# Performance work log

Hardware: AMD Instinct MI355X
Metric: run time of the kernel (lower is better)

Reference implementation:

```python
import jax, jax.numpy as jnp
import numpy as np

# ---- constants matching init_kwargs ----
NUM_CLASSES = 20
NUM_GRID = 7
NUM_BBOX = 2
IN_SIZE = 448          # image_shapes = (448, 448)
IOU_THRESHOLD = 0.7    # self.num_threshold passed to batched_nms
SCORE_THRESHOLD = 0.1  # boxes[:, -1] > 0.1 reserve mask
M = NUM_GRID * NUM_GRID  # 49 boxes per image
BATCH = 16384


def setup_inputs() -> dict:
    key = jax.random.key(0)
    out_features = M * (NUM_CLASSES + 5 * NUM_BBOX)  # 1470
    x = jax.random.uniform(key, (BATCH, out_features), dtype=jnp.float32)
    return {"x": x}


def _iou_matrix(boxes):
    # boxes: [M, 4] in (x0, y0, x1, y1). Returns [M, M] pairwise IoU.
    area = jnp.clip(boxes[:, 2] - boxes[:, 0], 0) * jnp.clip(boxes[:, 3] - boxes[:, 1], 0)
    lt = jnp.maximum(boxes[:, None, :2], boxes[None, :, :2])   # [M, M, 2]
    rb = jnp.minimum(boxes[:, None, 2:], boxes[None, :, 2:])   # [M, M, 2]
    wh = jnp.clip(rb - lt, 0)
    inter = wh[..., 0] * wh[..., 1]
    union = area[:, None] + area[None, :] - inter
    return inter / jnp.maximum(union, 1e-9)


def _nms_keep(boxes, scores, labels, valid):
    # Per-image class-aware NMS (torchvision batched_nms semantics via coordinate offsets).
    # boxes [M,4], scores [M], labels [M] int, valid [M] bool -> keep mask [M] bool.
    max_coord = jnp.max(boxes)
    offs = labels.astype(boxes.dtype) * (max_coord + 1.0)
    b = boxes + offs[:, None]
    s = jnp.where(valid, scores, -jnp.inf)
    order = jnp.argsort(-s)                 # descending by score, invalid last
    bs = b[order]
    vs = valid[order]
    iou = _iou_matrix(bs)                   # [M, M]
    idx = jnp.arange(M)

    def step(suppressed, i):
        keep_i = vs[i] & ~suppressed[i]
        suppressed = suppressed | (keep_i & (iou[i] > IOU_THRESHOLD) & (idx > i))
        return suppressed, keep_i

    _, keep_sorted = jax.lax.scan(step, jnp.zeros((M,), bool), idx)
    return jnp.zeros((M,), bool).at[order].set(keep_sorted)


def reference(x):
    N = x.shape[0]
    x = x.reshape(N, M, NUM_CLASSES + 5 * NUM_BBOX)
    class_logits = x[..., :NUM_CLASSES]                       # [N, M, C]
    bb = x[..., NUM_CLASSES:].reshape(N, M, NUM_BBOX, 5)      # [N, M, B, 5]
    # pick the bbox with max confidence per cell
    best = jnp.argmax(bb[..., 4], axis=-1)                    # [N, M]
    yolo_bboxes = jnp.take_along_axis(bb, best[..., None, None], axis=2)[:, :, 0, :]  # [N, M, 5]

    probs = jax.nn.softmax(class_logits, axis=-1)
    labels = jnp.argmax(probs, axis=-1)                       # [N, M]

    # boxes_decode: grid offsets (x tiles, y repeats) then cx/cy/w/h -> corners
    g = jnp.arange(NUM_GRID, dtype=x.dtype)
    x_grid = jnp.tile(g, NUM_GRID)                            # [M]
    y_grid = jnp.repeat(g, NUM_GRID)                          # [M]
    cx = (yolo_bboxes[..., 0] + x_grid) / NUM_GRID
    cy = (yolo_bboxes[..., 1] + y_grid) / NUM_GRID
    hw = yolo_bboxes[..., 2] / 2
    hh = yolo_bboxes[..., 3] / 2
    W = jnp.asarray(IN_SIZE, x.dtype)
    H = jnp.asarray(IN_SIZE, x.dtype)
    x0 = (cx - hw) * W
    y0 = (cy - hh) * H
    x1 = (cx + hw) * W
    y1 = (cy + hh) * H
    scores = yolo_bboxes[..., 4]
    reserve_mask = scores > SCORE_THRESHOLD                   # [N, M]

    # clip_boxes_to_image
    x0 = jnp.clip(x0, 0, IN_SIZE); x1 = jnp.clip(x1, 0, IN_SIZE)
    y0 = jnp.clip(y0, 0, IN_SIZE); y1 = jnp.clip(y1, 0, IN_SIZE)
    boxes = jnp.stack([x0, y0, x1, y1], axis=-1)              # [N, M, 4]

    keep_mask = jax.vmap(_nms_keep)(boxes, scores, labels, reserve_mask)  # [N, M]
    return class_logits, yolo_bboxes, boxes, scores, labels, keep_mask, reserve_mask
```

## Files before the change

### kernel.cpp

```cpp
#include <hip/hip_runtime.h>
#include <math.h>

#define NCLS   20
#define MCELLS 49
#define FEAT   30
#define ITEMF  1470

typedef unsigned long long u64;
typedef unsigned int u32;
typedef float f32x4 __attribute__((ext_vector_type(4)));

__device__ __forceinline__ void nts(float* p, float v) { __builtin_nontemporal_store(v, p); }
__device__ __forceinline__ float bperm(int srcLane, float v) {
  return __int_as_float(__builtin_amdgcn_ds_bpermute(srcLane << 2, __float_as_int(v)));
}

__global__ __launch_bounds__(256) void yolo_post(const float* __restrict__ x,
                                                 float* __restrict__ out,
                                                 int N) {
  const int wave = threadIdx.x >> 6;
  const int lane = threadIdx.x & 63;
  const int n = blockIdx.x * 4 + wave;
  if (n >= N) return;

  const float* item = x + (size_t)n * ITEMF;

  const size_t NM = (size_t)N * MCELLS;
  float* out0 = out;
  float* out1 = out0 + NM * 20;
  float* out2 = out1 + NM * 5;
  float* out3 = out2 + NM * 4;
  float* out4 = out3 + NM;
  float* out5 = out4 + NM;
  float* out6 = out5 + NM;

  const int m = lane;
  const bool cellv = (m < MCELLS);

  float2 v[15];
  if (cellv) {
    const float2* Lp = (const float2*)(item + m * FEAT);
#pragma unroll
    for (int j = 0; j < 15; ++j) v[j] = Lp[j];
  } else {
#pragma unroll
    for (int j = 0; j < 15; ++j) v[j] = make_float2(0.f, 0.f);
  }

  {
    float* dst = out0 + (size_t)n * (MCELLS * NCLS);
#pragma unroll
    for (int i = 0; i < 16; ++i) {
      int idx = lane + i * 64;
      if (idx < MCELLS * NCLS) {
        int c = idx / NCLS;
        int k = idx - c * NCLS;
        nts(dst + idx, item[c * FEAT + k]);
      }
    }
  }

  int   labi = 0;
  float conf = 0.f;
  float x0 = 0.f, y0 = 0.f, x1 = 0.f, y1 = 0.f;
  bool  reserve = false;

  if (cellv) {
    float bestv = v[0].x;
    if (v[0].y > bestv) { bestv = v[0].y; labi = 1; }
#pragma unroll
    for (int j = 1; j < 10; ++j) {
      if (v[j].x > bestv) { bestv = v[j].x; labi = 2 * j; }
      if (v[j].y > bestv) { bestv = v[j].y; labi = 2 * j + 1; }
    }

    float c0 = v[12].x, c1 = v[14].y;
    bool sel1 = (c1 > c0);
    float bx = sel1 ? v[12].y : v[10].x;
    float by = sel1 ? v[13].x : v[10].y;
    float bw = sel1 ? v[13].y : v[11].x;
    float bh = sel1 ? v[14].x : v[11].y;
    conf = sel1 ? c1 : c0;

    float xg = (float)(m % 7), yg = (float)(m / 7);
    float cx = (bx + xg) / 7.0f, cy = (by + yg) / 7.0f;
    float hw = bw * 0.5f, hh = bh * 0.5f;
    x0 = fminf(fmaxf((cx - hw) * 448.0f, 0.f), 448.f);
    y0 = fminf(fmaxf((cy - hh) * 448.0f, 0.f), 448.f);
    x1 = fminf(fmaxf((cx + hw) * 448.0f, 0.f), 448.f);
    y1 = fminf(fmaxf((cy + hh) * 448.0f, 0.f), 448.f);
    reserve = (conf > 0.1f);

    size_t ci = (size_t)n * MCELLS + m;
    float* yb = out1 + ci * 5;
    nts(yb + 0, bx); nts(yb + 1, by); nts(yb + 2, bw); nts(yb + 3, bh); nts(yb + 4, conf);
    f32x4 bx4 = { x0, y0, x1, y1 };
    __builtin_nontemporal_store(bx4, (f32x4*)(out2 + ci * 4));
    nts(out3 + ci, conf);
    nts(out4 + ci, (float)labi);
    nts(out6 + ci, reserve ? 1.0f : 0.0f);
  }

  const bool meValid = (cellv && reserve);
  const u64 validb = __ballot(meValid);

  u64 same = ~0ull;
#pragma unroll
  for (int b = 0; b < 5; ++b) {
    u64 bb = __ballot(((labi >> b) & 1) != 0);
    same &= ((labi >> b) & 1) ? bb : ~bb;
  }
  u64 peers = same & validb & ~(1ull << lane);
  if (!meValid) peers = 0;

  int pc = __popcll(peers);
#pragma unroll
  for (int d = 1; d < 64; d <<= 1) {
    int o = __shfl_xor(pc, d);
    pc = pc > o ? pc : o;
  }
  const int T = __builtin_amdgcn_readfirstlane(pc);

  const float area_i = fmaxf(x1 - x0, 0.f) * fmaxf(y1 - y0, 0.f);
  u64 candme = 0;
  u64 rem = peers;
  for (int t = 0; t < T; ++t) {
    int j = rem ? (int)__builtin_ctzll(rem) : lane;
    rem &= rem - 1;
    float cj  = bperm(j, conf);
    float jx0 = bperm(j, x0), jy0 = bperm(j, y0);
    float jx1 = bperm(j, x1), jy1 = bperm(j, y1);
    bool prec = (cj > conf) || ((cj == conf) && (j < lane));
    float aj = fmaxf(jx1 - jx0, 0.f) * fmaxf(jy1 - jy0, 0.f);
    float iw = fminf(jx1, x1) - fmaxf(jx0, x0);
    float ih = fminf(jy1, y1) - fmaxf(jy0, y0);
    float inter = fmaxf(iw, 0.f) * fmaxf(ih, 0.f);
    float uni = aj + area_i - inter;
    bool sup = prec && (inter > 0.7f * fmaxf(uni, 1e-9f));
    candme |= sup ? (1ull << j) : 0ull;
  }

  u64 undecided = validb, kept = 0;
  while (undecided) {
    bool meUnd  = meValid && ((undecided >> lane) & 1ull);
    bool ready  = meUnd && ((candme & undecided) == 0ull);
    u64 readyb  = __ballot(ready);
    u64 keptb   = __ballot(ready && ((candme & kept) == 0ull));
    kept |= keptb;
    undecided &= ~readyb;
  }

  if (cellv) nts(out5 + (size_t)n * MCELLS + m, (float)((kept >> lane) & 1ull));
}

extern "C" void kernel_launch(void* const* d_in, const int* in_sizes, int n_in,
                              void* d_out, int out_size, void* d_ws, size_t ws_size,
                              hipStream_t stream) {
  const float* x = (const float*)d_in[0];
  float* out = (float*)d_out;
  int N = in_sizes[0] / ITEMF;
  int grid = (N + 3) / 4;
  yolo_post<<<grid, 256, 0, stream>>>(x, out, N);
}
```

Measured before the change: 40.52 us.

## Process four images per wave with double-buffered register prefetch

Each wave now handles four images instead of one. The per-cell loads for the next image are issued into a second register buffer before the current image is processed. This is meant to hide global-load latency behind the NMS and store work, and to cut the number of waves launched. In exchange it raises register pressure, which may lower occupancy, and leaves a quarter as many waves to spread across the GPU. Lanes 49 and above no longer zero-initialise the item buffer, but those values are never used.

```diff
diff --git a/kernel.cpp b/kernel.cpp
--- a/kernel.cpp
+++ b/kernel.cpp
@@ -5,6 +5,7 @@
 #define MCELLS 49
 #define FEAT   30
 #define ITEMF  1470
+#define IPW    4
 
 typedef unsigned long long u64;
 typedef unsigned int u32;
@@ -15,37 +16,26 @@
   return __int_as_float(__builtin_amdgcn_ds_bpermute(srcLane << 2, __float_as_int(v)));
 }
 
-__global__ __launch_bounds__(256) void yolo_post(const float* __restrict__ x,
-                                                 float* __restrict__ out,
-                                                 int N) {
-  const int wave = threadIdx.x >> 6;
-  const int lane = threadIdx.x & 63;
-  const int n = blockIdx.x * 4 + wave;
+struct Item { float2 v[15]; };
+
+__device__ __forceinline__ void loadItem(Item& it, const float* __restrict__ x,
+                                         long n, int N, bool cellv, int m) {
+  if ((n < N) && cellv) {
+    const float2* Lp = (const float2*)(x + (size_t)n * ITEMF + m * FEAT);
+#pragma unroll
+    for (int j = 0; j < 15; ++j) it.v[j] = Lp[j];
+  }
+}
+
+__device__ __forceinline__ void processItem(const Item& it, long n, int N, int lane,
+                                            const float* __restrict__ x,
+                                            float* out0, float* out1, float* out2,
+                                            float* out3, float* out4, float* out5,
+                                            float* out6) {
   if (n >= N) return;
-
-  const float* item = x + (size_t)n * ITEMF;
-
-  const size_t NM = (size_t)N * MCELLS;
-  float* out0 = out;
-  float* out1 = out0 + NM * 20;
-  float* out2 = out1 + NM * 5;
-  float* out3 = out2 + NM * 4;
-  float* out4 = out3 + NM;
-  float* out5 = out4 + NM;
-  float* out6 = out5 + NM;
-
   const int m = lane;
   const bool cellv = (m < MCELLS);
-
-  float2 v[15];
-  if (cellv) {
-    const float2* Lp = (const float2*)(item + m * FEAT);
-#pragma unroll
-    for (int j = 0; j < 15; ++j) v[j] = Lp[j];
-  } else {
-#pragma unroll
-    for (int j = 0; j < 15; ++j) v[j] = make_float2(0.f, 0.f);
-  }
+  const float* item = x + (size_t)n * ITEMF;
 
   {
     float* dst = out0 + (size_t)n * (MCELLS * NCLS);
@@ -66,20 +56,20 @@
   bool  reserve = false;
 
   if (cellv) {
-    float bestv = v[0].x;
-    if (v[0].y > bestv) { bestv = v[0].y; labi = 1; }
+    float bestv = it.v[0].x;
+    if (it.v[0].y > bestv) { bestv = it.v[0].y; labi = 1; }
 #pragma unroll
     for (int j = 1; j < 10; ++j) {
-      if (v[j].x > bestv) { bestv = v[j].x; labi = 2 * j; }
-      if (v[j].y > bestv) { bestv = v[j].y; labi = 2 * j + 1; }
+      if (it.v[j].x > bestv) { bestv = it.v[j].x; labi = 2 * j; }
+      if (it.v[j].y > bestv) { bestv = it.v[j].y; labi = 2 * j + 1; }
     }
 
-    float c0 = v[12].x, c1 = v[14].y;
+    float c0 = it.v[12].x, c1 = it.v[14].y;
     bool sel1 = (c1 > c0);
-    float bx = sel1 ? v[12].y : v[10].x;
-    float by = sel1 ? v[13].x : v[10].y;
-    float bw = sel1 ? v[13].y : v[11].x;
-    float bh = sel1 ? v[14].x : v[11].y;
+    float bx = sel1 ? it.v[12].y : it.v[10].x;
+    float by = sel1 ? it.v[13].x : it.v[10].y;
+    float bw = sel1 ? it.v[13].y : it.v[11].x;
+    float bh = sel1 ? it.v[14].x : it.v[11].y;
     conf = sel1 ? c1 : c0;
 
     float xg = (float)(m % 7), yg = (float)(m / 7);
@@ -153,12 +143,45 @@
   if (cellv) nts(out5 + (size_t)n * MCELLS + m, (float)((kept >> lane) & 1ull));
 }
 
+__global__ __launch_bounds__(256) void yolo_post(const float* __restrict__ x,
+                                                 float* __restrict__ out,
+                                                 int N) {
+  const int wave = threadIdx.x >> 6;
+  const int lane = threadIdx.x & 63;
+  const int gw = blockIdx.x * 4 + wave;
+  const long i0 = (long)gw * IPW;
+  if (i0 >= N) return;
+
+  const int m = lane;
+  const bool cellv = (m < MCELLS);
+
+  const size_t NM = (size_t)N * MCELLS;
+  float* out0 = out;
+  float* out1 = out0 + NM * 20;
+  float* out2 = out1 + NM * 5;
+  float* out3 = out2 + NM * 4;
+  float* out4 = out3 + NM;
+  float* out5 = out4 + NM;
+  float* out6 = out5 + NM;
+
+  Item A, B;
+  loadItem(A, x, i0 + 0, N, cellv, m);
+  loadItem(B, x, i0 + 1, N, cellv, m);
+  processItem(A, i0 + 0, N, lane, x, out0, out1, out2, out3, out4, out5, out6);
+  loadItem(A, x, i0 + 2, N, cellv, m);
+  processItem(B, i0 + 1, N, lane, x, out0, out1, out2, out3, out4, out5, out6);
+  loadItem(B, x, i0 + 3, N, cellv, m);
+  processItem(A, i0 + 2, N, lane, x, out0, out1, out2, out3, out4, out5, out6);
+  processItem(B, i0 + 3, N, lane, x, out0, out1, out2, out3, out4, out5, out6);
+}
+
 extern "C" void kernel_launch(void* const* d_in, const int* in_sizes, int n_in,
                               void* d_out, int out_size, void* d_ws, size_t ws_size,
                               hipStream_t stream) {
   const float* x = (const float*)d_in[0];
   float* out = (float*)d_out;
   int N = in_sizes[0] / ITEMF;
-  int grid = (N + 3) / 4;
+  int waves = (N + IPW - 1) / IPW;
+  int grid = (waves + 3) / 4;
   yolo_post<<<grid, 256, 0, stream>>>(x, out, N);
 }
```

After: 50.42 us. 1.24x slower.

## Split into streaming decode kernel and separate NMS kernel, stage logits via LDS

Applied to the files above, without the earlier changes.

Splits the single fused kernel into two. The first streams the input, writes the outputs and stages class logits through shared memory so they are copied from registers rather than re-read from global memory. The second kernel reloads the boxes, scores and labels from the output buffer (regular stores so they stay in cache) and runs the NMS. The goal is to keep the bandwidth-bound phase free of the divergent NMS loops. In exchange it adds a second launch and an extra read pass over the box, score and label data, and the shared-memory staging relies only on a block-level fence within the wave.

```diff
diff --git a/kernel.cpp b/kernel.cpp
--- a/kernel.cpp
+++ b/kernel.cpp
@@ -15,15 +15,16 @@
   return __int_as_float(__builtin_amdgcn_ds_bpermute(srcLane << 2, __float_as_int(v)));
 }
 
-__global__ __launch_bounds__(256) void yolo_post(const float* __restrict__ x,
-                                                 float* __restrict__ out,
-                                                 int N) {
+__global__ __launch_bounds__(256) void yolo_stream(const float* __restrict__ x,
+                                                   float* __restrict__ out,
+                                                   int N) {
   const int wave = threadIdx.x >> 6;
   const int lane = threadIdx.x & 63;
   const int n = blockIdx.x * 4 + wave;
+
+  __shared__ float slog[4][MCELLS * NCLS];
+
   if (n >= N) return;
-
-  const float* item = x + (size_t)n * ITEMF;
 
   const size_t NM = (size_t)N * MCELLS;
   float* out0 = out;
@@ -31,15 +32,14 @@
   float* out2 = out1 + NM * 5;
   float* out3 = out2 + NM * 4;
   float* out4 = out3 + NM;
-  float* out5 = out4 + NM;
-  float* out6 = out5 + NM;
+  float* out6 = out4 + NM * 2;
 
   const int m = lane;
   const bool cellv = (m < MCELLS);
 
   float2 v[15];
   if (cellv) {
-    const float2* Lp = (const float2*)(item + m * FEAT);
+    const float2* Lp = (const float2*)(x + (size_t)n * ITEMF + m * FEAT);
 #pragma unroll
     for (int j = 0; j < 15; ++j) v[j] = Lp[j];
   } else {
@@ -47,25 +47,24 @@
     for (int j = 0; j < 15; ++j) v[j] = make_float2(0.f, 0.f);
   }
 
+  if (cellv) {
+    float2* dst = (float2*)&slog[wave][m * NCLS];
+#pragma unroll
+    for (int j = 0; j < 10; ++j) dst[j] = v[j];
+  }
+  __threadfence_block();
   {
     float* dst = out0 + (size_t)n * (MCELLS * NCLS);
+    const float* s = slog[wave];
 #pragma unroll
     for (int i = 0; i < 16; ++i) {
       int idx = lane + i * 64;
-      if (idx < MCELLS * NCLS) {
-        int c = idx / NCLS;
-        int k = idx - c * NCLS;
-        nts(dst + idx, item[c * FEAT + k]);
-      }
+      if (idx < MCELLS * NCLS) nts(dst + idx, s[idx]);
     }
   }
 
-  int   labi = 0;
-  float conf = 0.f;
-  float x0 = 0.f, y0 = 0.f, x1 = 0.f, y1 = 0.f;
-  bool  reserve = false;
-
   if (cellv) {
+    int labi = 0;
     float bestv = v[0].x;
     if (v[0].y > bestv) { bestv = v[0].y; labi = 1; }
 #pragma unroll
@@ -80,26 +79,52 @@
     float by = sel1 ? v[13].x : v[10].y;
     float bw = sel1 ? v[13].y : v[11].x;
     float bh = sel1 ? v[14].x : v[11].y;
-    conf = sel1 ? c1 : c0;
+    float conf = sel1 ? c1 : c0;
 
     float xg = (float)(m % 7), yg = (float)(m / 7);
     float cx = (bx + xg) / 7.0f, cy = (by + yg) / 7.0f;
     float hw = bw * 0.5f, hh = bh * 0.5f;
-    x0 = fminf(fmaxf((cx - hw) * 448.0f, 0.f), 448.f);
-    y0 = fminf(fmaxf((cy - hh) * 448.0f, 0.f), 448.f);
-    x1 = fminf(fmaxf((cx + hw) * 448.0f, 0.f), 448.f);
-    y1 = fminf(fmaxf((cy + hh) * 448.0f, 0.f), 448.f);
-    reserve = (conf > 0.1f);
+    float x0 = fminf(fmaxf((cx - hw) * 448.0f, 0.f), 448.f);
+    float y0 = fminf(fmaxf((cy - hh) * 448.0f, 0.f), 448.f);
+    float x1 = fminf(fmaxf((cx + hw) * 448.0f, 0.f), 448.f);
+    float y1 = fminf(fmaxf((cy + hh) * 448.0f, 0.f), 448.f);
 
     size_t ci = (size_t)n * MCELLS + m;
     float* yb = out1 + ci * 5;
     nts(yb + 0, bx); nts(yb + 1, by); nts(yb + 2, bw); nts(yb + 3, bh); nts(yb + 4, conf);
     f32x4 bx4 = { x0, y0, x1, y1 };
-    __builtin_nontemporal_store(bx4, (f32x4*)(out2 + ci * 4));
-    nts(out3 + ci, conf);
-    nts(out4 + ci, (float)labi);
-    nts(out6 + ci, reserve ? 1.0f : 0.0f);
+    *(f32x4*)(out2 + ci * 4) = bx4;
+    out3[ci] = conf;
+    out4[ci] = (float)labi;
+    nts(out6 + ci, (conf > 0.1f) ? 1.0f : 0.0f);
   }
+}
+
+__global__ __launch_bounds__(256) void yolo_nms(float* __restrict__ out, int N) {
+  const int wave = threadIdx.x >> 6;
+  const int lane = threadIdx.x & 63;
+  const int n = blockIdx.x * 4 + wave;
+  if (n >= N) return;
+
+  const size_t NM = (size_t)N * MCELLS;
+  const float* out2 = out + NM * 25;
+  const float* out3 = out + NM * 29;
+  const float* out4 = out + NM * 30;
+  float* out5 = out + NM * 31;
+
+  const int m = lane;
+  const bool cellv = (m < MCELLS);
+  const size_t ci = (size_t)n * MCELLS + m;
+
+  float x0 = 0.f, y0 = 0.f, x1 = 0.f, y1 = 0.f, conf = 0.f;
+  int labi = 0;
+  if (cellv) {
+    f32x4 b = *(const f32x4*)(out2 + ci * 4);
+    x0 = b.x; y0 = b.y; x1 = b.z; y1 = b.w;
+    conf = out3[ci];
+    labi = (int)out4[ci];
+  }
+  const bool reserve = (conf > 0.1f);
 
   const bool meValid = (cellv && reserve);
   const u64 validb = __ballot(meValid);
@@ -150,7 +175,7 @@
     undecided &= ~readyb;
   }
 
-  if (cellv) nts(out5 + (size_t)n * MCELLS + m, (float)((kept >> lane) & 1ull));
+  if (cellv) nts(out5 + ci, (float)((kept >> lane) & 1ull));
 }
 
 extern "C" void kernel_launch(void* const* d_in, const int* in_sizes, int n_in,
@@ -160,5 +185,6 @@
   float* out = (float*)d_out;
   int N = in_sizes[0] / ITEMF;
   int grid = (N + 3) / 4;
-  yolo_post<<<grid, 256, 0, stream>>>(x, out, N);
+  yolo_stream<<<grid, 256, 0, stream>>>(x, out, N);
+  yolo_nms<<<grid, 256, 0, stream>>>(out, N);
 }
```

Result: slower. 48.90 us (+20.7%).
